# Kernel tuning notes

Measured on AMD Instinct MI355X. Metric: run time of the kernel, lower is better.

Reference implementation:

```python
import jax, jax.numpy as jnp
import numpy as np

NGRID, NLAYER = 8192, 24
NPERIODS, NOBS, NC = 50, 4096, 200
SIGMA = 1.0
VREF = 3.0          # reference crustal Vs (km/s) for depth-sensitivity scale
RAYLEIGH_FACTOR = 0.92


def setup_inputs() -> dict:
    key = jax.random.key(0)
    k1, k2, k3 = jax.random.split(key, 3)
    # S-wave velocity model, 2.0-4.0 km/s, flattened as in log_prob(Vs_flat)
    Vs_flat = (2.0 + 2.0 * jax.random.uniform(k1, (NGRID, NLAYER))).reshape(-1).astype(jnp.float32)
    # Ray-path averaging matrix: nonnegative, rows sum to 1 (slowness average)
    A = jax.random.uniform(k2, (NOBS, NGRID), dtype=jnp.float32)
    A = A / A.sum(axis=1, keepdims=True)
    # Beamforming energy spectra per observation pair: (Nobs, Nperiods, Nc)
    energy = jax.random.uniform(k3, (NOBS, NPERIODS, NC), dtype=jnp.float32)
    # Monotone phase-velocity axis per observation: (Nobs, Nc)
    c_axis = jnp.zeros((NOBS, NC), jnp.float32) + jnp.linspace(1.5, 5.0, NC, dtype=jnp.float32)
    thick = jnp.full((NLAYER,), 2.0, jnp.float32)          # 2 km layers
    periods = jnp.linspace(1.0, 60.0, NPERIODS, dtype=jnp.float32)
    return {"Vs_flat": Vs_flat, "A": A, "energy": energy, "c_axis": c_axis,
            "thick": thick, "periods": periods}


def _dispersion_all_cells(Vs, thick, periods):
    # Differentiable surrogate for the batched surf96 forward across all grid cells.
    # Vs: (G, L), thick: (L,), periods: (P,)  ->  c_true: (G, P)
    z = jnp.cumsum(thick) - 0.5 * thick                      # layer-center depths (L,)
    depth_scale = VREF * periods / 3.0                       # ~ sensing depth per period (P,)
    w = jnp.exp(-z[None, :] / depth_scale[:, None]) * thick[None, :]  # (P, L)
    w = w / w.sum(axis=1, keepdims=True)
    return RAYLEIGH_FACTOR * jnp.einsum('pl,gl->gp', w, Vs)  # (G, P)


def reference(Vs_flat, A, energy, c_axis, thick, periods):
    Vs = Vs_flat.reshape(NGRID, NLAYER)
    c_true = _dispersion_all_cells(Vs, thick, periods)       # (Ngrid, Nperiods)
    # _apply_A: slowness averaging along ray paths
    s_pred = A @ (1.0 / c_true)                              # (Nobs, Nperiods)
    c_pred = 1.0 / s_pred
    # _interp1d_torch, vectorized over all (obs, period) pairs
    idx = jax.vmap(jnp.searchsorted)(c_axis, c_pred)         # (Nobs, Nperiods)
    idx = jnp.clip(idx, 1, NC - 1)
    c0 = jnp.take_along_axis(c_axis, idx - 1, axis=1)
    c1 = jnp.take_along_axis(c_axis, idx, axis=1)
    e0 = jnp.take_along_axis(energy, (idx - 1)[:, :, None], axis=2)[..., 0]
    e1 = jnp.take_along_axis(energy, idx[:, :, None], axis=2)[..., 0]
    w = (c_pred - c0) / (c1 - c0 + 1e-12)
    e_interp = e0 + w * (e1 - e0)
    e_max = energy.max(axis=-1)                              # (Nobs, Nperiods)
    log_like = -jnp.sum(e_max - e_interp) / (SIGMA ** 2)
    return log_like
```

## Files before the change

### kernel.cpp

```cpp
#include <hip/hip_runtime.h>

#define NGRID 8192
#define NLAYER 24
#define NPERIODS 50
#define NOBS 4096
#define NC 200
#define PP 64
#define NSPLIT 8
#define NBINS 1024
#define OTILE 64
#define KG 32
#define VREF 3.0f

__global__ void k0_zero(float* __restrict__ bins) {
    bins[threadIdx.x] = 0.f;
}

__global__ __launch_bounds__(256) void k1_rpad(const float* __restrict__ Vs,
                                               const float* __restrict__ thick,
                                               const float* __restrict__ periods,
                                               float* __restrict__ r_pad) {
    __shared__ float w_sh[NLAYER][NPERIODS];
    __shared__ float z_sh[NLAYER];
    int tid = threadIdx.x;
    if (tid < NLAYER) {
        float c = 0.f;
        for (int i = 0; i <= tid; ++i) c += thick[i];
        z_sh[tid] = c - 0.5f * thick[tid];
    }
    __syncthreads();
    if (tid < NPERIODS) {
        float ds = (VREF / 3.0f) * periods[tid];
        float tmp[NLAYER];
        float s = 0.f;
        #pragma unroll
        for (int l = 0; l < NLAYER; ++l) {
            float v = expf(-z_sh[l] / ds) * thick[l];
            tmp[l] = v; s += v;
        }
        float inv = 1.f / s;
        #pragma unroll
        for (int l = 0; l < NLAYER; ++l) w_sh[l][tid] = tmp[l] * inv;
    }
    __syncthreads();
    int idx = blockIdx.x * 256 + tid;
    int g = idx >> 6, p = idx & 63;
    float r = 0.f;
    if (p < NPERIODS) {
        const float4* vp = (const float4*)(Vs + (size_t)g * NLAYER);
        float s = 0.f;
        #pragma unroll
        for (int q = 0; q < NLAYER / 4; ++q) {
            float4 t = vp[q];
            s = fmaf(w_sh[4*q+0][p], t.x, s);
            s = fmaf(w_sh[4*q+1][p], t.y, s);
            s = fmaf(w_sh[4*q+2][p], t.z, s);
            s = fmaf(w_sh[4*q+3][p], t.w, s);
        }
        r = 1.0f / (0.92f * s);
    }
    r_pad[idx] = r;
}

__global__ __launch_bounds__(256) void k2_gemm(const float* __restrict__ A,
                                               const float* __restrict__ r_pad,
                                               float* __restrict__ partial) {
    __shared__ float lds[4 * OTILE * 36];
    int tid  = threadIdx.x;
    int lane = tid & 63;
    int wv   = __builtin_amdgcn_readfirstlane(tid >> 6);
    int o_base = blockIdx.x * OTILE;
    int split  = blockIdx.y;
    float* Aw = lds + wv * (OTILE * 36);

    float acc[NPERIODS];
    #pragma unroll
    for (int p = 0; p < NPERIODS; ++p) acc[p] = 0.f;

    const int GC = NGRID / (NSPLIT * 4);
    int g_wave = (split * 4 + wv) * GC;

    for (int kt = 0; kt < GC / KG; ++kt) {
        int g0 = g_wave + kt * KG;
        #pragma unroll
        for (int s = 0; s < 8; ++s) {
            int f   = s * 64 + lane;
            int row = f >> 3;
            int c4  = (f & 7) * 4;
            float4 t = *(const float4*)(A + (size_t)(o_base + row) * NGRID + g0 + c4);
            *(float4*)(Aw + row * 36 + c4) = t;
        }
        __syncthreads();
        #pragma unroll 1
        for (int gg = 0; gg < KG; gg += 4) {
            float4 a4 = *(const float4*)(Aw + lane * 36 + gg);
            const float* rr = r_pad + (size_t)(g0 + gg) * PP;
            #pragma unroll
            for (int j = 0; j < 4; ++j) {
                float aj = (j == 0) ? a4.x : (j == 1) ? a4.y : (j == 2) ? a4.z : a4.w;
                const float* rj = rr + j * PP;
                #pragma unroll
                for (int p = 0; p < NPERIODS; ++p) acc[p] = fmaf(aj, rj[p], acc[p]);
            }
        }
        __syncthreads();
    }

    float* outp = partial + (size_t)split * (NOBS * PP) + (size_t)o_base * PP;
    #pragma unroll
    for (int h = 0; h < 2; ++h) {
        __syncthreads();
        float* rw = lds + wv * (OTILE * 33);
        #pragma unroll
        for (int q = 0; q < 32; ++q) {
            int p = h * 32 + q;
            rw[lane * 33 + q] = (p < NPERIODS) ? acc[p] : 0.f;
        }
        __syncthreads();
        for (int e = tid; e < OTILE * 32; e += 256) {
            int oo = e >> 5, q = e & 31;
            float v = 0.f;
            #pragma unroll
            for (int w2 = 0; w2 < 4; ++w2) v += lds[w2 * (OTILE * 33) + oo * 33 + q];
            outp[oo * PP + h * 32 + q] = v;
        }
    }
}

__global__ __launch_bounds__(256) void k3_main(const float* __restrict__ energy,
                                               const float* __restrict__ c_axis,
                                               const float* __restrict__ partial,
                                               float* __restrict__ bins) {
    __shared__ float red[4];
    int tid  = threadIdx.x;
    int lane = tid & 63;
    int wv   = tid >> 6;
    int pair = blockIdx.x * 4 + wv;
    int o = pair / NPERIODS;
    int p = pair - o * NPERIODS;

    float sp = 0.f;
    if (lane < NSPLIT) sp = partial[(size_t)lane * (NOBS * PP) + (size_t)o * PP + p];
    #pragma unroll
    for (int m = 32; m; m >>= 1) sp += __shfl_xor(sp, m, 64);
    float cp = 1.0f / sp;

    const float* erow = energy + ((size_t)o * NPERIODS + p) * NC;
    const float* crow = c_axis + (size_t)o * NC;
    float cnt = 0.f, mx = -1e30f;
    if (lane < NC / 4) {
        float4 e  = *(const float4*)(erow + 4 * lane);
        float4 ca = *(const float4*)(crow + 4 * lane);
        mx  = fmaxf(fmaxf(e.x, e.y), fmaxf(e.z, e.w));
        cnt = (ca.x < cp ? 1.f : 0.f) + (ca.y < cp ? 1.f : 0.f)
            + (ca.z < cp ? 1.f : 0.f) + (ca.w < cp ? 1.f : 0.f);
    }
    #pragma unroll
    for (int m = 32; m; m >>= 1) {
        cnt += __shfl_xor(cnt, m, 64);
        mx   = fmaxf(mx, __shfl_xor(mx, m, 64));
    }
    int idx = (int)cnt;
    idx = idx < 1 ? 1 : (idx > NC - 1 ? NC - 1 : idx);
    float c0 = crow[idx - 1], c1 = crow[idx];
    float e0 = erow[idx - 1], e1 = erow[idx];
    float wgt = (cp - c0) / (c1 - c0 + 1e-12f);
    float ei  = fmaf(wgt, e1 - e0, e0);
    float contrib = mx - ei;

    if (lane == 0) red[wv] = contrib;
    __syncthreads();
    if (tid == 0)
        atomicAdd(&bins[blockIdx.x & (NBINS - 1)], red[0] + red[1] + red[2] + red[3]);
}

__global__ __launch_bounds__(256) void k4_final(const float* __restrict__ bins,
                                                float* __restrict__ out) {
    __shared__ float red[4];
    int tid = threadIdx.x;
    float s = 0.f;
    for (int i = tid; i < NBINS; i += 256) s += bins[i];
    #pragma unroll
    for (int m = 32; m; m >>= 1) s += __shfl_xor(s, m, 64);
    int lane = tid & 63, wv = tid >> 6;
    if (lane == 0) red[wv] = s;
    __syncthreads();
    if (tid == 0) out[0] = -(red[0] + red[1] + red[2] + red[3]);
}

extern "C" void kernel_launch(void* const* d_in, const int* in_sizes, int n_in,
                              void* d_out, int out_size, void* d_ws, size_t ws_size,
                              hipStream_t stream) {
    const float* Vs      = (const float*)d_in[0];
    const float* A       = (const float*)d_in[1];
    const float* energy  = (const float*)d_in[2];
    const float* c_axis  = (const float*)d_in[3];
    const float* thick   = (const float*)d_in[4];
    const float* periods = (const float*)d_in[5];
    float* out = (float*)d_out;

    float* ws      = (float*)d_ws;
    float* r_pad   = ws;
    float* partial = r_pad + (size_t)NGRID * PP;
    float* bins    = partial + (size_t)NSPLIT * NOBS * PP;

    hipLaunchKernelGGL(k0_zero, dim3(1), dim3(NBINS), 0, stream, bins);
    hipLaunchKernelGGL(k1_rpad, dim3((NGRID * PP) / 256), dim3(256), 0, stream,
                       Vs, thick, periods, r_pad);
    hipLaunchKernelGGL(k2_gemm, dim3(NOBS / OTILE, NSPLIT), dim3(256), 0, stream,
                       A, r_pad, partial);
    hipLaunchKernelGGL(k3_main, dim3((NOBS * NPERIODS) / 4), dim3(256), 0, stream,
                       energy, c_axis, partial, bins);
    hipLaunchKernelGGL(k4_final, dim3(1), dim3(256), 0, stream, bins, out);
}
```

Measured before the change: 424.3 us.

## Widen GEMM split-K with 8-wave blocks, add reduce kernel, restructure interp per observation

The GEMM kernel now uses 512-thread blocks with 8 waves, 16 splits over the grid dimension and smaller K tiles, so more waves are in flight. The block-wide barriers inside the K loop are removed because each wave only touches its own LDS tile. A separate kernel sums the split partials and inverts them into c_pred, and the interpolation kernel now runs one block per observation, staging c_axis in LDS and looping over periods. Partial outputs are stored compactly with 50 periods instead of padded to 64, at the cost of one extra launch and more partial traffic from the doubled split count.

```diff
diff --git a/kernel.cpp b/kernel.cpp
--- a/kernel.cpp
+++ b/kernel.cpp
@@ -6,10 +6,13 @@
 #define NOBS 4096
 #define NC 200
 #define PP 64
-#define NSPLIT 8
+#define NSPLIT 16
+#define WPB 8
+#define GC 64
+#define KG 16
+#define LDSTR 20
 #define NBINS 1024
 #define OTILE 64
-#define KG 32
 #define VREF 3.0f
 
 __global__ void k0_zero(float* __restrict__ bins) {
@@ -62,38 +65,37 @@
     r_pad[idx] = r;
 }
 
-__global__ __launch_bounds__(256) void k2_gemm(const float* __restrict__ A,
-                                               const float* __restrict__ r_pad,
-                                               float* __restrict__ partial) {
-    __shared__ float lds[4 * OTILE * 36];
+__global__ __launch_bounds__(512, 8) void k2_gemm(const float* __restrict__ A,
+                                                  const float* __restrict__ r_pad,
+                                                  float* __restrict__ partial) {
+    __shared__ float lds[WPB * OTILE * LDSTR];
     int tid  = threadIdx.x;
     int lane = tid & 63;
     int wv   = __builtin_amdgcn_readfirstlane(tid >> 6);
     int o_base = blockIdx.x * OTILE;
     int split  = blockIdx.y;
-    float* Aw = lds + wv * (OTILE * 36);
+    float* Aw = lds + wv * (OTILE * LDSTR);
 
     float acc[NPERIODS];
     #pragma unroll
     for (int p = 0; p < NPERIODS; ++p) acc[p] = 0.f;
 
-    const int GC = NGRID / (NSPLIT * 4);
-    int g_wave = (split * 4 + wv) * GC;
-
+    int g_wave = (split * WPB + wv) * GC;
+
+    #pragma unroll 1
     for (int kt = 0; kt < GC / KG; ++kt) {
         int g0 = g_wave + kt * KG;
         #pragma unroll
-        for (int s = 0; s < 8; ++s) {
+        for (int s = 0; s < 4; ++s) {
             int f   = s * 64 + lane;
-            int row = f >> 3;
-            int c4  = (f & 7) * 4;
+            int row = f >> 2;
+            int c4  = (f & 3) * 4;
             float4 t = *(const float4*)(A + (size_t)(o_base + row) * NGRID + g0 + c4);
-            *(float4*)(Aw + row * 36 + c4) = t;
-        }
-        __syncthreads();
+            *(float4*)(Aw + row * LDSTR + c4) = t;
+        }
         #pragma unroll 1
         for (int gg = 0; gg < KG; gg += 4) {
-            float4 a4 = *(const float4*)(Aw + lane * 36 + gg);
+            float4 a4 = *(const float4*)(Aw + lane * LDSTR + gg);
             const float* rr = r_pad + (size_t)(g0 + gg) * PP;
             #pragma unroll
             for (int j = 0; j < 4; ++j) {
@@ -103,72 +105,89 @@
                 for (int p = 0; p < NPERIODS; ++p) acc[p] = fmaf(aj, rj[p], acc[p]);
             }
         }
+    }
+
+    float* outp = partial + (size_t)split * (NOBS * NPERIODS) + (size_t)o_base * NPERIODS;
+    #pragma unroll 1
+    for (int h = 0; h < 4; ++h) {
         __syncthreads();
-    }
-
-    float* outp = partial + (size_t)split * (NOBS * PP) + (size_t)o_base * PP;
-    #pragma unroll
-    for (int h = 0; h < 2; ++h) {
+        float* rw = lds + wv * (OTILE * 17);
+        #pragma unroll
+        for (int q = 0; q < 16; ++q) {
+            int p = h * 16 + q;
+            rw[lane * 17 + q] = (p < NPERIODS) ? acc[p] : 0.f;
+        }
         __syncthreads();
-        float* rw = lds + wv * (OTILE * 33);
-        #pragma unroll
-        for (int q = 0; q < 32; ++q) {
-            int p = h * 32 + q;
-            rw[lane * 33 + q] = (p < NPERIODS) ? acc[p] : 0.f;
-        }
-        __syncthreads();
-        for (int e = tid; e < OTILE * 32; e += 256) {
-            int oo = e >> 5, q = e & 31;
-            float v = 0.f;
-            #pragma unroll
-            for (int w2 = 0; w2 < 4; ++w2) v += lds[w2 * (OTILE * 33) + oo * 33 + q];
-            outp[oo * PP + h * 32 + q] = v;
-        }
-    }
+        for (int e = tid; e < OTILE * 16; e += 512) {
+            int oo = e >> 4, q = e & 15;
+            int p  = h * 16 + q;
+            if (p < NPERIODS) {
+                float v = 0.f;
+                #pragma unroll
+                for (int w2 = 0; w2 < WPB; ++w2) v += lds[w2 * (OTILE * 17) + oo * 17 + q];
+                outp[oo * NPERIODS + p] = v;
+            }
+        }
+    }
+}
+
+__global__ __launch_bounds__(256) void k2b_reduce(const float* __restrict__ partial,
+                                                  float* __restrict__ cpred) {
+    int idx = blockIdx.x * 256 + threadIdx.x;
+    int o = idx >> 6, p = idx & 63;
+    float v = 0.f;
+    if (p < NPERIODS) {
+        float s = 0.f;
+        #pragma unroll
+        for (int sp = 0; sp < NSPLIT; ++sp)
+            s += partial[(size_t)sp * (NOBS * NPERIODS) + (size_t)o * NPERIODS + p];
+        v = 1.0f / s;
+    }
+    cpred[idx] = v;
 }
 
 __global__ __launch_bounds__(256) void k3_main(const float* __restrict__ energy,
                                                const float* __restrict__ c_axis,
-                                               const float* __restrict__ partial,
+                                               const float* __restrict__ cpred,
                                                float* __restrict__ bins) {
+    __shared__ float csh[NC];
     __shared__ float red[4];
     int tid  = threadIdx.x;
     int lane = tid & 63;
     int wv   = tid >> 6;
-    int pair = blockIdx.x * 4 + wv;
-    int o = pair / NPERIODS;
-    int p = pair - o * NPERIODS;
-
-    float sp = 0.f;
-    if (lane < NSPLIT) sp = partial[(size_t)lane * (NOBS * PP) + (size_t)o * PP + p];
-    #pragma unroll
-    for (int m = 32; m; m >>= 1) sp += __shfl_xor(sp, m, 64);
-    float cp = 1.0f / sp;
-
-    const float* erow = energy + ((size_t)o * NPERIODS + p) * NC;
-    const float* crow = c_axis + (size_t)o * NC;
-    float cnt = 0.f, mx = -1e30f;
-    if (lane < NC / 4) {
-        float4 e  = *(const float4*)(erow + 4 * lane);
-        float4 ca = *(const float4*)(crow + 4 * lane);
-        mx  = fmaxf(fmaxf(e.x, e.y), fmaxf(e.z, e.w));
-        cnt = (ca.x < cp ? 1.f : 0.f) + (ca.y < cp ? 1.f : 0.f)
-            + (ca.z < cp ? 1.f : 0.f) + (ca.w < cp ? 1.f : 0.f);
-    }
-    #pragma unroll
-    for (int m = 32; m; m >>= 1) {
-        cnt += __shfl_xor(cnt, m, 64);
-        mx   = fmaxf(mx, __shfl_xor(mx, m, 64));
-    }
-    int idx = (int)cnt;
-    idx = idx < 1 ? 1 : (idx > NC - 1 ? NC - 1 : idx);
-    float c0 = crow[idx - 1], c1 = crow[idx];
-    float e0 = erow[idx - 1], e1 = erow[idx];
-    float wgt = (cp - c0) / (c1 - c0 + 1e-12f);
-    float ei  = fmaf(wgt, e1 - e0, e0);
-    float contrib = mx - ei;
-
-    if (lane == 0) red[wv] = contrib;
+    int o    = blockIdx.x;
+
+    if (tid < NC) csh[tid] = c_axis[(size_t)o * NC + tid];
+    __syncthreads();
+
+    float4 ca = make_float4(0.f, 0.f, 0.f, 0.f);
+    if (lane < NC / 4) ca = *(const float4*)(csh + 4 * lane);
+
+    float local = 0.f;
+    for (int p = wv; p < NPERIODS; p += 4) {
+        float cp = cpred[(size_t)o * PP + p];
+        const float* erow = energy + ((size_t)o * NPERIODS + p) * NC;
+        float mx = -1e30f, cnt = 0.f;
+        if (lane < NC / 4) {
+            float4 e = *(const float4*)(erow + 4 * lane);
+            mx  = fmaxf(fmaxf(e.x, e.y), fmaxf(e.z, e.w));
+            cnt = (ca.x < cp ? 1.f : 0.f) + (ca.y < cp ? 1.f : 0.f)
+                + (ca.z < cp ? 1.f : 0.f) + (ca.w < cp ? 1.f : 0.f);
+        }
+        #pragma unroll
+        for (int m = 32; m; m >>= 1) {
+            cnt += __shfl_xor(cnt, m, 64);
+            mx   = fmaxf(mx, __shfl_xor(mx, m, 64));
+        }
+        int idx = (int)cnt;
+        idx = idx < 1 ? 1 : (idx > NC - 1 ? NC - 1 : idx);
+        float c0 = csh[idx - 1], c1 = csh[idx];
+        float e0 = erow[idx - 1], e1 = erow[idx];
+        float w  = (cp - c0) / (c1 - c0 + 1e-12f);
+        float ei = fmaf(w, e1 - e0, e0);
+        local += mx - ei;
+    }
+    if (lane == 0) red[wv] = local;
     __syncthreads();
     if (tid == 0)
         atomicAdd(&bins[blockIdx.x & (NBINS - 1)], red[0] + red[1] + red[2] + red[3]);
@@ -202,14 +221,17 @@
     float* ws      = (float*)d_ws;
     float* r_pad   = ws;
     float* partial = r_pad + (size_t)NGRID * PP;
-    float* bins    = partial + (size_t)NSPLIT * NOBS * PP;
+    float* cpred   = partial + (size_t)NSPLIT * NOBS * NPERIODS;
+    float* bins    = cpred + (size_t)NOBS * PP;
 
     hipLaunchKernelGGL(k0_zero, dim3(1), dim3(NBINS), 0, stream, bins);
     hipLaunchKernelGGL(k1_rpad, dim3((NGRID * PP) / 256), dim3(256), 0, stream,
                        Vs, thick, periods, r_pad);
-    hipLaunchKernelGGL(k2_gemm, dim3(NOBS / OTILE, NSPLIT), dim3(256), 0, stream,
+    hipLaunchKernelGGL(k2_gemm, dim3(NOBS / OTILE, NSPLIT), dim3(512), 0, stream,
                        A, r_pad, partial);
-    hipLaunchKernelGGL(k3_main, dim3((NOBS * NPERIODS) / 4), dim3(256), 0, stream,
-                       energy, c_axis, partial, bins);
+    hipLaunchKernelGGL(k2b_reduce, dim3((NOBS * PP) / 256), dim3(256), 0, stream,
+                       partial, cpred);
+    hipLaunchKernelGGL(k3_main, dim3(NOBS), dim3(256), 0, stream,
+                       energy, c_axis, cpred, bins);
     hipLaunchKernelGGL(k4_final, dim3(1), dim3(256), 0, stream, bins, out);
 }
```

Result: slower. 470.3 us (+10.9%).
